# Kernel optimization log

Measured on AMD Instinct MI355X. Metric: run time of the kernel, lower is better.

## Reference

```python
import jax, jax.numpy as jnp
import numpy as np
import math

N_HEADS = 16
HEAD_DIM = 64
ROPE_BASE = 10000.0


def _rope_tables(T, head_dim, dtype):
    inv_freq = 1.0 / (ROPE_BASE ** (jnp.arange(0, head_dim, 2, dtype=jnp.float32) / head_dim))
    t = jnp.arange(T, dtype=jnp.float32)
    freqs = jnp.outer(t, inv_freq)          # (T, head_dim/2)
    emb = jnp.concatenate([freqs, freqs], axis=-1)  # (T, head_dim)
    return jnp.cos(emb).astype(dtype), jnp.sin(emb).astype(dtype)


def _rotate_half(x):
    x1, x2 = jnp.split(x, 2, axis=-1)
    return jnp.concatenate([-x2, x1], axis=-1)


def setup_inputs() -> dict:
    key = jax.random.key(0)
    k1, k2, k3 = jax.random.split(key, 3)
    B, T, D = 2, 2048, 1024
    x = jax.random.normal(k1, (B, T, D), dtype=jnp.float32)
    W_qkv = jax.random.normal(k2, (D, 3 * D), dtype=jnp.float32) * (1.0 / math.sqrt(D))
    W_proj = jax.random.normal(k3, (D, D), dtype=jnp.float32) * (1.0 / math.sqrt(D))
    return {"x": x, "W_qkv": W_qkv, "W_proj": W_proj}


def reference(x, W_qkv, W_proj):
    B, T, C = x.shape
    H, Dh = N_HEADS, HEAD_DIM
    qkv = x @ W_qkv                                   # (B,T,3C)
    q, k, v = jnp.split(qkv, 3, axis=-1)
    # (B,T,C) -> (B,H,T,Dh)
    q = q.reshape(B, T, H, Dh).transpose(0, 2, 1, 3)
    k = k.reshape(B, T, H, Dh).transpose(0, 2, 1, 3)
    v = v.reshape(B, T, H, Dh).transpose(0, 2, 1, 3)
    cos, sin = _rope_tables(T, Dh, x.dtype)           # (T,Dh)
    q = q * cos + _rotate_half(q) * sin
    k = k * cos + _rotate_half(k) * sin
    scale = 1.0 / math.sqrt(Dh)
    att = jnp.einsum('bhqd,bhkd->bhqk', q, k) * scale
    causal = jnp.tril(jnp.ones((T, T), dtype=bool))
    att = jnp.where(causal, att, -jnp.inf)
    att = jax.nn.softmax(att, axis=-1)
    y = jnp.einsum('bhqk,bhkd->bhqd', att, v)         # (B,H,T,Dh)
    y = y.transpose(0, 2, 1, 3).reshape(B, T, C)
    return y @ W_proj
```

## Files before the change

### kernel.cpp

```cpp
#include <hip/hip_runtime.h>
#include <hip/hip_bf16.h>
#include <math.h>

typedef __bf16 bf16_t;
typedef __bf16 bf16x8 __attribute__((ext_vector_type(8)));
typedef __bf16 bf16x4 __attribute__((ext_vector_type(4)));
typedef __bf16 bf16x2 __attribute__((ext_vector_type(2)));
typedef float  f32x4  __attribute__((ext_vector_type(4)));
typedef float  f32x16 __attribute__((ext_vector_type(16)));

__device__ __forceinline__ void gload_lds16(const void* g, void* l) {
  __builtin_amdgcn_global_load_lds((const __attribute__((address_space(1))) void*)g,
                                   (__attribute__((address_space(3))) void*)l,
                                   16, 0, 0);
}

__device__ __forceinline__ unsigned pk2(float a, float b) {
  union { bf16x2 h; unsigned u; } x;
  x.h[0] = (bf16_t)a; x.h[1] = (bf16_t)b;
  return x.u;
}
__device__ __forceinline__ bf16x8 frag4(unsigned w0, unsigned w1, unsigned w2, unsigned w3) {
  union { unsigned u[4]; bf16x8 f; } x;
  x.u[0] = w0; x.u[1] = w1; x.u[2] = w2; x.u[3] = w3;
  return x.f;
}
__device__ __forceinline__ void pls(unsigned a, unsigned b, unsigned& x, unsigned& y) {
  auto rr = __builtin_amdgcn_permlane32_swap(a, b, false, false);
  x = ((unsigned*)&rr)[0];
  y = ((unsigned*)&rr)[1];
}

__global__ __launch_bounds__(256) void prep_all(const float* __restrict__ x,
                                                const float* __restrict__ Wqkv,
                                                const float* __restrict__ Wproj,
                                                bf16_t* __restrict__ xb,
                                                bf16_t* __restrict__ wqkvt,
                                                bf16_t* __restrict__ wprojt,
                                                float* __restrict__ cosT,
                                                float* __restrict__ sinT) {
  __shared__ float tile[32][33];
  int bx = blockIdx.x;
  if (bx < 4096) {
    int idx = (bx * 256 + threadIdx.x) * 4;
    float4 v = *(const float4*)(x + idx);
    bf16x4 o;
    o[0] = (bf16_t)v.x; o[1] = (bf16_t)v.y; o[2] = (bf16_t)v.z; o[3] = (bf16_t)v.w;
    *(bf16x4*)(xb + idx) = o;
  } else if (bx < 8192) {
    const float* W; bf16_t* Wt; int K, N, n0, k0;
    if (bx < 7168) {
      W = Wqkv; Wt = wqkvt; K = 1024; N = 3072;
      int b = bx - 4096; n0 = (b % 96) * 32; k0 = (b / 96) * 32;
    } else {
      W = Wproj; Wt = wprojt; K = 1024; N = 1024;
      int b = bx - 7168; n0 = (b & 31) * 32; k0 = (b >> 5) * 32;
    }
    int tx = threadIdx.x & 31, ty = threadIdx.x >> 5;
    #pragma unroll
    for (int i = 0; i < 4; ++i) {
      int k = ty + i * 8;
      tile[k][tx] = W[(size_t)(k0 + k) * N + n0 + tx];
    }
    __syncthreads();
    #pragma unroll
    for (int i = 0; i < 4; ++i) {
      int r = ty + i * 8;
      Wt[(size_t)(n0 + r) * K + k0 + tx] = (bf16_t)tile[tx][r];
    }
  } else {
    int b = bx - 8192;
    int t = b * 4 + (threadIdx.x >> 6);
    int d = threadIdx.x & 63;
    float inv = __expf(-logf(10000.f) * (float)(d & 31) * (1.f / 32.f));
    float ang = (float)t * inv;
    cosT[t * 64 + d] = cosf(ang);
    sinT[t * 64 + d] = sinf(ang);
  }
}

template <int OUT_BF16>
__global__ __launch_bounds__(256) void gemm_bt(const bf16_t* __restrict__ A,
                                               const bf16_t* __restrict__ Bt,
                                               void* __restrict__ Cout,
                                               int M, int N, int K) {
  const int tid = threadIdx.x;
  const int l = tid & 63, w = tid >> 6;
  const int lr = l & 15, lg = l >> 4;
  const int nwgx = gridDim.x, nwgy = gridDim.y;
  const int orig = blockIdx.y * nwgx + blockIdx.x;
  const int cpx = (nwgx * nwgy) >> 3;
  const int s_id = (orig & 7) * cpx + (orig >> 3);
  const int bx = s_id / nwgy;
  const int by = s_id % nwgy;
  const int wr = w >> 1, wc = w & 1;
  __shared__ __align__(16) bf16_t lA[128 * 64];
  __shared__ __align__(16) bf16_t lB[128 * 64];
  f32x4 acc[4][4];
  const f32x4 zf = {0.f, 0.f, 0.f, 0.f};
  #pragma unroll
  for (int m = 0; m < 4; ++m)
    #pragma unroll
    for (int n = 0; n < 4; ++n) acc[m][n] = zf;

  const int sr8 = l >> 3;
  const int sc16 = ((l & 7) * 16) ^ (sr8 << 4);
  const char* Ab = (const char*)(A + (size_t)(by * 128) * K);
  const char* Bb = (const char*)(Bt + (size_t)(bx * 128) * K);
  const size_t rowb = (size_t)K * 2;

  for (int k0 = 0; k0 < 2 * K; k0 += 128) {
    #pragma unroll
    for (int p = 0; p < 4; ++p) {
      int row = p * 32 + w * 8 + sr8;
      gload_lds16(Ab + (size_t)row * rowb + k0 + sc16, (char*)lA + p * 4096 + w * 1024);
      gload_lds16(Bb + (size_t)row * rowb + k0 + sc16, (char*)lB + p * 4096 + w * 1024);
    }
    __syncthreads();
    #pragma unroll
    for (int kk = 0; kk < 2; ++kk) {
      bf16x8 aF[4], bF[4];
      #pragma unroll
      for (int m = 0; m < 4; ++m) {
        int row = wr * 64 + m * 16 + lr;
        aF[m] = *(const bf16x8*)((const char*)lA + row * 128 +
                                 ((kk * 64 + lg * 16) ^ ((row & 7) << 4)));
      }
      #pragma unroll
      for (int n = 0; n < 4; ++n) {
        int row = wc * 64 + n * 16 + lr;
        bF[n] = *(const bf16x8*)((const char*)lB + row * 128 +
                                 ((kk * 64 + lg * 16) ^ ((row & 7) << 4)));
      }
      #pragma unroll
      for (int m = 0; m < 4; ++m)
        #pragma unroll
        for (int n = 0; n < 4; ++n)
          acc[m][n] = __builtin_amdgcn_mfma_f32_16x16x32_bf16(aF[m], bF[n], acc[m][n], 0, 0, 0);
    }
    __syncthreads();
  }

  const int orow0 = by * 128 + wr * 64;
  const int ocol0 = bx * 128 + wc * 64;
  if (OUT_BF16) {
    bf16_t* C = (bf16_t*)Cout;
    #pragma unroll
    for (int m = 0; m < 4; ++m)
      #pragma unroll
      for (int n = 0; n < 4; ++n)
        #pragma unroll
        for (int r = 0; r < 4; ++r)
          C[(size_t)(orow0 + m * 16 + lg * 4 + r) * N + ocol0 + n * 16 + lr] =
              (bf16_t)acc[m][n][r];
  } else {
    float* C = (float*)Cout;
    #pragma unroll
    for (int m = 0; m < 4; ++m)
      #pragma unroll
      for (int n = 0; n < 4; ++n)
        #pragma unroll
        for (int r = 0; r < 4; ++r)
          C[(size_t)(orow0 + m * 16 + lg * 4 + r) * N + ocol0 + n * 16 + lr] =
              acc[m][n][r];
  }
}

__global__ __launch_bounds__(256) void prep_qkv(const bf16_t* __restrict__ qkv,
                                                const float* __restrict__ cosT,
                                                const float* __restrict__ sinT,
                                                bf16_t* __restrict__ Q,
                                                bf16_t* __restrict__ Kr,
                                                bf16_t* __restrict__ VT) {
  __shared__ __align__(16) bf16_t tile[64][72];
  int bx = blockIdx.x;
  if (bx < 16384) {
    int gid = bx * 4 + (threadIdx.x >> 6);
    int d = threadIdx.x & 63;
    int t = gid & 2047, bh = gid >> 11;
    int b = bh >> 4, h = bh & 15;
    const bf16_t* row = qkv + (size_t)(b * 2048 + t) * 3072 + h * 64;
    float q = (float)row[d];
    float k = (float)row[1024 + d];
    float c = cosT[t * 64 + d], s = sinT[t * 64 + d];
    float qp = __shfl_xor(q, 32);
    float kp = __shfl_xor(k, 32);
    float qr = (d < 32) ? -qp : qp;
    float krot = (d < 32) ? -kp : kp;
    size_t o = ((size_t)bh * 2048 + t) * 64 + d;
    Q[o] = (bf16_t)((q * c + qr * s) * 0.18033688011112042f);
    Kr[o] = (bf16_t)(k * c + krot * s);
  } else {
    int b2 = bx - 16384;
    int bh = b2 & 31, b = bh >> 4, h = bh & 15;
    int t0 = (b2 >> 5) * 64;
    int r = threadIdx.x >> 2, c4 = threadIdx.x & 3;
    const bf16_t* src = qkv + (size_t)(b * 2048 + t0 + r) * 3072 + 2048 + h * 64 + c4 * 16;
    *(bf16x8*)&tile[r][c4 * 16] = *(const bf16x8*)src;
    *(bf16x8*)&tile[r][c4 * 16 + 8] = *(const bf16x8*)(src + 8);
    __syncthreads();
    bf16x8 v0, v1;
    #pragma unroll
    for (int i = 0; i < 8; ++i) v0[i] = tile[c4 * 16 + i][r];
    #pragma unroll
    for (int i = 0; i < 8; ++i) v1[i] = tile[c4 * 16 + 8 + i][r];
    bf16_t* dst = VT + ((size_t)bh * 64 + r) * 2048 + t0 + c4 * 16;
    *(bf16x8*)dst = v0;
    *(bf16x8*)(dst + 8) = v1;
  }
}

__global__ __launch_bounds__(512, 4) void attn(const bf16_t* __restrict__ Q,
                                               const bf16_t* __restrict__ K,
                                               const bf16_t* __restrict__ VT,
                                               bf16_t* __restrict__ Y) {
  const int L = blockIdx.x;
  const int bh = L & 31;
  const int idx = (L & 255) >> 5;
  const int qi = (L >= 256) ? (15 - 2 * idx) : (2 * idx);
  const int b = bh >> 4, h = bh & 15;
  const int tid = threadIdx.x, l = tid & 63, w = tid >> 6;
  const int qw = w & 3, half = w >> 2;
  const int tid2 = tid & 255;
  const int l31 = l & 31, hi = l >> 5;
  const int hi4 = hi * 4, hi8 = hi * 8;
  const int qbase = qi * 128 + qw * 32;
  const int qown = qbase + l31;
  const int ntile = qi + 1;
  const int t0 = half * ntile, tend = t0 + ntile;
  const int tdiag = qbase >> 6;

  __shared__ __align__(16) char smem[65536];
  char* Kbase = smem + half * 16384;
  char* Vbase = smem + 32768 + half * 16384;

  const bf16_t* Qb = Q + (size_t)bh * 2048 * 64;
  const bf16_t* Kb0 = K + (size_t)bh * 2048 * 64;
  const bf16_t* Vb = VT + (size_t)bh * 64 * 2048;

  bf16x8 qf[4];
  #pragma unroll
  for (int kk = 0; kk < 4; ++kk)
    qf[kk] = *(const bf16x8*)(Qb + (size_t)qown * 64 + kk * 16 + hi8);

  const int srow = tid2 >> 3;
  const int scolb = (tid2 & 7) * 16;
  const int rA = srow, rB = 32 + srow;
  const int swA = scolb ^ ((rA & 7) << 4);
  const int swB = scolb ^ ((rB & 7) << 4);
  const char* KgA = (const char*)Kb0 + (size_t)t0 * 8192 + (size_t)rA * 128 + swA;
  const char* KgB = (const char*)Kb0 + (size_t)t0 * 8192 + (size_t)rB * 128 + swB;
  const char* VgA = (const char*)Vb + (size_t)t0 * 128 + (size_t)rA * 4096 + swA;
  const char* VgB = (const char*)Vb + (size_t)t0 * 128 + (size_t)rB * 4096 + swB;

  f32x16 oa[2];
  #pragma unroll
  for (int dt = 0; dt < 2; ++dt)
    #pragma unroll
    for (int r = 0; r < 16; ++r) oa[dt][r] = 0.f;
  float lacc0 = 0.f, lacc1 = 0.f;

  gload_lds16(KgA, Kbase + tid2 * 16);
  gload_lds16(KgB, Kbase + 4096 + tid2 * 16);
  gload_lds16(VgA, Vbase + tid2 * 16);
  gload_lds16(VgB, Vbase + 4096 + tid2 * 16);
  KgA += 8192; KgB += 8192; VgA += 128; VgB += 128;
  __syncthreads();

  int cur = 0;
  for (int t = t0; t < tend; ++t) {
    if (t + 1 < tend) {
      char* dK = Kbase + (cur ^ 1) * 8192;
      char* dV = Vbase + (cur ^ 1) * 8192;
      gload_lds16(KgA, dK + tid2 * 16);
      gload_lds16(KgB, dK + 4096 + tid2 * 16);
      gload_lds16(VgA, dV + tid2 * 16);
      gload_lds16(VgB, dV + 4096 + tid2 * 16);
      KgA += 8192; KgB += 8192; VgA += 128; VgB += 128;
    }
    const char* KlH = Kbase + cur * 8192;
    const char* VlH = Vbase + cur * 8192;

    if (t <= tdiag) {
      f32x16 s[2];
      #pragma unroll
      for (int sb = 0; sb < 2; ++sb)
        #pragma unroll
        for (int r = 0; r < 16; ++r) s[sb][r] = 0.f;
      __builtin_amdgcn_s_setprio(1);
      #pragma unroll
      for (int sb = 0; sb < 2; ++sb) {
        int row = sb * 32 + l31;
        const char* kr = KlH + row * 128;
        int sw = (row & 7) << 4;
        #pragma unroll
        for (int kk = 0; kk < 4; ++kk) {
          bf16x8 kf = *(const bf16x8*)(kr + ((kk * 32 + hi * 16) ^ sw));
          s[sb] = __builtin_amdgcn_mfma_f32_32x32x16_bf16(kf, qf[kk], s[sb], 0, 0, 0);
        }
      }
      __builtin_amdgcn_s_setprio(0);

      if (t == tdiag) {
        #pragma unroll
        for (int sb = 0; sb < 2; ++sb)
          #pragma unroll
          for (int r = 0; r < 16; ++r) {
            int kv = t * 64 + sb * 32 + (r & 3) + 8 * (r >> 2) + hi4;
            if (kv > qown) s[sb][r] = -__builtin_inff();
          }
      }

      #pragma unroll
      for (int r = 0; r < 16; ++r) {
        float p0 = exp2f(s[0][r]);
        float p1 = exp2f(s[1][r]);
        s[0][r] = p0; lacc0 += p0;
        s[1][r] = p1; lacc1 += p1;
      }

      #pragma unroll
      for (int sb = 0; sb < 2; ++sb) {
        unsigned a0 = pk2(s[sb][0], s[sb][1]),   a1 = pk2(s[sb][2], s[sb][3]);
        unsigned b0 = pk2(s[sb][4], s[sb][5]),   b1 = pk2(s[sb][6], s[sb][7]);
        unsigned c0 = pk2(s[sb][8], s[sb][9]),   c1 = pk2(s[sb][10], s[sb][11]);
        unsigned d0 = pk2(s[sb][12], s[sb][13]), d1 = pk2(s[sb][14], s[sb][15]);
        unsigned r0x, r0y, r1x, r1y, r2x, r2y, r3x, r3y;
        pls(a0, b0, r0x, r0y);
        pls(a1, b1, r1x, r1y);
        pls(c0, d0, r2x, r2y);
        pls(c1, d1, r3x, r3y);
        bf16x8 pf0 = frag4(r0x, r1x, r0y, r1y);
        bf16x8 pf1 = frag4(r2x, r3x, r2y, r3y);
        __builtin_amdgcn_s_setprio(1);
        #pragma unroll
        for (int kk = 0; kk < 2; ++kk) {
          bf16x8 pf = kk ? pf1 : pf0;
          #pragma unroll
          for (int dt = 0; dt < 2; ++dt) {
            int vrow = dt * 32 + l31;
            const char* vr = VlH + vrow * 128;
            bf16x8 vf = *(const bf16x8*)(vr + ((sb * 64 + kk * 32 + hi * 16) ^ ((vrow & 7) << 4)));
            oa[dt] = __builtin_amdgcn_mfma_f32_32x32x16_bf16(vf, pf, oa[dt], 0, 0, 0);
          }
        }
        __builtin_amdgcn_s_setprio(0);
      }
    }

    __syncthreads();
    cur ^= 1;
  }

  float lacc = lacc0 + lacc1;
  lacc += __shfl_xor(lacc, 32);
  float* OLDS = (float*)smem;
  float* LLDS = (float*)(smem + 32768);
  if (half == 1) {
    #pragma unroll
    for (int r = 0; r < 32; ++r)
      OLDS[r * 256 + qw * 64 + l] = oa[r >> 4][r & 15];
    LLDS[qw * 64 + l] = lacc;
  }
  __syncthreads();
  if (half == 0) {
    #pragma unroll
    for (int r = 0; r < 32; ++r)
      oa[r >> 4][r & 15] += OLDS[r * 256 + qw * 64 + l];
    float inv = 1.f / (lacc + LLDS[qw * 64 + l]);
    bf16_t* Yb = Y + (size_t)b * 2048 * 1024 + (size_t)qown * 1024 + h * 64;
    #pragma unroll
    for (int dt = 0; dt < 2; ++dt)
      #pragma unroll
      for (int g = 0; g < 4; ++g) {
        bf16x4 v;
        #pragma unroll
        for (int jj = 0; jj < 4; ++jj) v[jj] = (bf16_t)(oa[dt][g * 4 + jj] * inv);
        *(bf16x4*)(Yb + dt * 32 + g * 8 + hi4) = v;
      }
  }
}

extern "C" void kernel_launch(void* const* d_in, const int* in_sizes, int n_in,
                              void* d_out, int out_size, void* d_ws, size_t ws_size,
                              hipStream_t stream) {
  const float* x = (const float*)d_in[0];
  const float* Wqkv = (const float*)d_in[1];
  const float* Wproj = (const float*)d_in[2];
  float* out = (float*)d_out;
  char* ws = (char*)d_ws;

  bf16_t* xb     = (bf16_t*)(ws + (0u));
  bf16_t* wqkvt  = (bf16_t*)(ws + (8u << 20));
  bf16_t* wprojt = (bf16_t*)(ws + (14u << 20));
  bf16_t* qkv    = (bf16_t*)(ws + (16u << 20));
  bf16_t* Q      = (bf16_t*)(ws + (40u << 20));
  bf16_t* Kr     = (bf16_t*)(ws + (48u << 20));
  bf16_t* VT     = (bf16_t*)(ws + (56u << 20));
  bf16_t* Y      = (bf16_t*)(ws + (64u << 20));
  float*  cosT   = (float*)(ws + (72u << 20));
  float*  sinT   = (float*)(ws + (72u << 20) + (1u << 19));

  prep_all<<<dim3(8704), dim3(256), 0, stream>>>(x, Wqkv, Wproj, xb, wqkvt, wprojt, cosT, sinT);
  gemm_bt<1><<<dim3(24, 32), dim3(256), 0, stream>>>(xb, wqkvt, (void*)qkv, 4096, 3072, 1024);
  prep_qkv<<<dim3(17408), dim3(256), 0, stream>>>(qkv, cosT, sinT, Q, Kr, VT);
  attn<<<dim3(512), dim3(512), 0, stream>>>(Q, Kr, VT, Y);
  gemm_bt<0><<<dim3(8, 32), dim3(256), 0, stream>>>(Y, wprojt, (void*)out, 4096, 1024, 1024);
}
```

Baseline: 116.0 us.

## Fuse RoPE, Q scaling and head-major scatter into QKV GEMM epilogue

New measurement: 112.5 us, median of 2. 1.03x faster.

```diff
diff --git a/kernel.cpp b/kernel.cpp
--- a/kernel.cpp
+++ b/kernel.cpp
@@ -37,8 +37,7 @@
                                                 bf16_t* __restrict__ xb,
                                                 bf16_t* __restrict__ wqkvt,
                                                 bf16_t* __restrict__ wprojt,
-                                                float* __restrict__ cosT,
-                                                float* __restrict__ sinT) {
+                                                float2* __restrict__ csT) {
   __shared__ float tile[32][33];
   int bx = blockIdx.x;
   if (bx < 4096) {
@@ -74,15 +73,19 @@
     int d = threadIdx.x & 63;
     float inv = __expf(-logf(10000.f) * (float)(d & 31) * (1.f / 32.f));
     float ang = (float)t * inv;
-    cosT[t * 64 + d] = cosf(ang);
-    sinT[t * 64 + d] = sinf(ang);
-  }
-}
-
-template <int OUT_BF16>
+    float2 cs; cs.x = cosf(ang); cs.y = sinf(ang);
+    csT[t * 64 + d] = cs;
+  }
+}
+
+template <int MODE>
 __global__ __launch_bounds__(256) void gemm_bt(const bf16_t* __restrict__ A,
                                                const bf16_t* __restrict__ Bt,
                                                void* __restrict__ Cout,
+                                               const float2* __restrict__ csT,
+                                               bf16_t* __restrict__ Qo,
+                                               bf16_t* __restrict__ Ko,
+                                               bf16_t* __restrict__ Vt,
                                                int M, int N, int K) {
   const int tid = threadIdx.x;
   const int l = tid & 63, w = tid >> 6;
@@ -142,18 +145,8 @@
   }
 
   const int orow0 = by * 128 + wr * 64;
-  const int ocol0 = bx * 128 + wc * 64;
-  if (OUT_BF16) {
-    bf16_t* C = (bf16_t*)Cout;
-    #pragma unroll
-    for (int m = 0; m < 4; ++m)
-      #pragma unroll
-      for (int n = 0; n < 4; ++n)
-        #pragma unroll
-        for (int r = 0; r < 4; ++r)
-          C[(size_t)(orow0 + m * 16 + lg * 4 + r) * N + ocol0 + n * 16 + lr] =
-              (bf16_t)acc[m][n][r];
-  } else {
+  if (MODE == 0) {
+    const int ocol0 = bx * 128 + wc * 64;
     float* C = (float*)Cout;
     #pragma unroll
     for (int m = 0; m < 4; ++m)
@@ -163,51 +156,55 @@
         for (int r = 0; r < 4; ++r)
           C[(size_t)(orow0 + m * 16 + lg * 4 + r) * N + ocol0 + n * 16 + lr] =
               acc[m][n][r];
-  }
-}
-
-__global__ __launch_bounds__(256) void prep_qkv(const bf16_t* __restrict__ qkv,
-                                                const float* __restrict__ cosT,
-                                                const float* __restrict__ sinT,
-                                                bf16_t* __restrict__ Q,
-                                                bf16_t* __restrict__ Kr,
-                                                bf16_t* __restrict__ VT) {
+  } else {
+    const int region = bx >> 3;
+    const int h = ((bx & 7) << 1) + wc;
+    bf16_t* dst = (region == 0) ? Qo : ((region == 1) ? Ko : Vt);
+    const float qsc = (region == 0) ? 0.18033688011112042f : 1.0f;
+    #pragma unroll
+    for (int m = 0; m < 4; ++m)
+      #pragma unroll
+      for (int r = 0; r < 4; ++r) {
+        int grow = orow0 + m * 16 + lg * 4 + r;
+        int bb = grow >> 11, t = grow & 2047;
+        bf16_t* drow = dst + (((size_t)(bb * 16 + h) * 2048 + t) << 6);
+        if (region < 2) {
+          #pragma unroll
+          for (int n = 0; n < 4; ++n) {
+            int d = n * 16 + lr;
+            float2 cs = csT[t * 64 + d];
+            float v = acc[m][n][r];
+            float pv = acc[m][n ^ 2][r];
+            float rot = (n < 2) ? -pv : pv;
+            drow[d] = (bf16_t)((v * cs.x + rot * cs.y) * qsc);
+          }
+        } else {
+          #pragma unroll
+          for (int n = 0; n < 4; ++n)
+            drow[n * 16 + lr] = (bf16_t)acc[m][n][r];
+        }
+      }
+  }
+}
+
+__global__ __launch_bounds__(256) void prep_vt(const bf16_t* __restrict__ Vtmp,
+                                               bf16_t* __restrict__ VT) {
+  int bh = blockIdx.x & 31;
+  int t0 = (blockIdx.x >> 5) * 64;
   __shared__ __align__(16) bf16_t tile[64][72];
-  int bx = blockIdx.x;
-  if (bx < 16384) {
-    int gid = bx * 4 + (threadIdx.x >> 6);
-    int d = threadIdx.x & 63;
-    int t = gid & 2047, bh = gid >> 11;
-    int b = bh >> 4, h = bh & 15;
-    const bf16_t* row = qkv + (size_t)(b * 2048 + t) * 3072 + h * 64;
-    float q = (float)row[d];
-    float k = (float)row[1024 + d];
-    float c = cosT[t * 64 + d], s = sinT[t * 64 + d];
-    float qp = __shfl_xor(q, 32);
-    float kp = __shfl_xor(k, 32);
-    float qr = (d < 32) ? -qp : qp;
-    float krot = (d < 32) ? -kp : kp;
-    size_t o = ((size_t)bh * 2048 + t) * 64 + d;
-    Q[o] = (bf16_t)((q * c + qr * s) * 0.18033688011112042f);
-    Kr[o] = (bf16_t)(k * c + krot * s);
-  } else {
-    int b2 = bx - 16384;
-    int bh = b2 & 31, b = bh >> 4, h = bh & 15;
-    int t0 = (b2 >> 5) * 64;
-    int r = threadIdx.x >> 2, c4 = threadIdx.x & 3;
-    const bf16_t* src = qkv + (size_t)(b * 2048 + t0 + r) * 3072 + 2048 + h * 64 + c4 * 16;
-    *(bf16x8*)&tile[r][c4 * 16] = *(const bf16x8*)src;
-    *(bf16x8*)&tile[r][c4 * 16 + 8] = *(const bf16x8*)(src + 8);
-    __syncthreads();
-    bf16x8 v0, v1;
-    #pragma unroll
-    for (int i = 0; i < 8; ++i) v0[i] = tile[c4 * 16 + i][r];
-    #pragma unroll
-    for (int i = 0; i < 8; ++i) v1[i] = tile[c4 * 16 + 8 + i][r];
-    bf16_t* dst = VT + ((size_t)bh * 64 + r) * 2048 + t0 + c4 * 16;
-    *(bf16x8*)dst = v0;
-    *(bf16x8*)(dst + 8) = v1;
-  }
+  int r = threadIdx.x >> 2, c4 = threadIdx.x & 3;
+  const bf16_t* src = Vtmp + ((size_t)bh * 2048 + t0 + r) * 64 + c4 * 16;
+  *(bf16x8*)&tile[r][c4 * 16] = *(const bf16x8*)src;
+  *(bf16x8*)&tile[r][c4 * 16 + 8] = *(const bf16x8*)(src + 8);
+  __syncthreads();
+  bf16x8 v0, v1;
+  #pragma unroll
+  for (int i = 0; i < 8; ++i) v0[i] = tile[c4 * 16 + i][r];
+  #pragma unroll
+  for (int i = 0; i < 8; ++i) v1[i] = tile[c4 * 16 + 8 + i][r];
+  bf16_t* dst = VT + ((size_t)bh * 64 + r) * 2048 + t0 + c4 * 16;
+  *(bf16x8*)dst = v0;
+  *(bf16x8*)(dst + 8) = v1;
 }
 
 __global__ __launch_bounds__(512, 4) void attn(const bf16_t* __restrict__ Q,
@@ -393,17 +390,19 @@
   bf16_t* xb     = (bf16_t*)(ws + (0u));
   bf16_t* wqkvt  = (bf16_t*)(ws + (8u << 20));
   bf16_t* wprojt = (bf16_t*)(ws + (14u << 20));
-  bf16_t* qkv    = (bf16_t*)(ws + (16u << 20));
+  bf16_t* Vtmp   = (bf16_t*)(ws + (16u << 20));
   bf16_t* Q      = (bf16_t*)(ws + (40u << 20));
   bf16_t* Kr     = (bf16_t*)(ws + (48u << 20));
   bf16_t* VT     = (bf16_t*)(ws + (56u << 20));
   bf16_t* Y      = (bf16_t*)(ws + (64u << 20));
-  float*  cosT   = (float*)(ws + (72u << 20));
-  float*  sinT   = (float*)(ws + (72u << 20) + (1u << 19));
-
-  prep_all<<<dim3(8704), dim3(256), 0, stream>>>(x, Wqkv, Wproj, xb, wqkvt, wprojt, cosT, sinT);
-  gemm_bt<1><<<dim3(24, 32), dim3(256), 0, stream>>>(xb, wqkvt, (void*)qkv, 4096, 3072, 1024);
-  prep_qkv<<<dim3(17408), dim3(256), 0, stream>>>(qkv, cosT, sinT, Q, Kr, VT);
+  float2* csT    = (float2*)(ws + (72u << 20));
+
+  prep_all<<<dim3(8704), dim3(256), 0, stream>>>(x, Wqkv, Wproj, xb, wqkvt, wprojt, csT);
+  gemm_bt<1><<<dim3(24, 32), dim3(256), 0, stream>>>(xb, wqkvt, nullptr, csT, Q, Kr, Vtmp,
+                                                     4096, 3072, 1024);
+  prep_vt<<<dim3(1024), dim3(256), 0, stream>>>(Vtmp, VT);
   attn<<<dim3(512), dim3(512), 0, stream>>>(Q, Kr, VT, Y);
-  gemm_bt<0><<<dim3(8, 32), dim3(256), 0, stream>>>(Y, wprojt, (void*)out, 4096, 1024, 1024);
-}
+  gemm_bt<0><<<dim3(8, 32), dim3(256), 0, stream>>>(Y, wprojt, (void*)out, nullptr,
+                                                    nullptr, nullptr, nullptr,
+                                                    4096, 1024, 1024);
+}
```
